# Kernel optimization log

Measured on AMD Instinct MI355X. Metric: run time of the kernel, lower is better.

The kernel has to match this reference:

```python
import jax, jax.numpy as jnp
import numpy as np

# spk_param = (thr, temp, damp); dt, tau from module config
THR, TEMP, DAMP = 0.4, 0.1, 0.9
DT, TAU = 0.1, 1.0


@jax.custom_vjp
def spike(v, u):
    # Stochastic Bernoulli spike: sigmoid(temp*v) > uniform noise
    return (jax.nn.sigmoid(TEMP * v) > u).astype(v.dtype)

def _spike_fwd(v, u):
    return spike(v, u), v

def _spike_bwd(v, g):
    # Faithful to the torch Spike.backward: returns the pseudo-derivative
    # damp*clamp(1-|v|,0) directly (the original ignores grad_output).
    return (DAMP * jnp.maximum(1.0 - jnp.abs(v), 0.0), jnp.zeros_like(v))

spike.defvjp(_spike_fwd, _spike_bwd)


def setup_inputs() -> dict:
    key = jax.random.key(0)
    k1, k2, k3, k4, k5 = jax.random.split(key, 5)
    B_, T, IN, N, OUT = 128, 512, 128, 512, 128
    inputs = jax.random.normal(k1, (B_, T, IN), dtype=jnp.float32)
    rand_u = jax.random.uniform(k2, (B_, T, N), dtype=jnp.float32)
    init_std = 1.0
    J = jax.random.normal(k3, (N, N), dtype=jnp.float32) * (init_std / np.sqrt(N))
    Bw = jax.random.normal(k4, (N, IN), dtype=jnp.float32)  # input projection (non-trainable in torch)
    W = jax.random.normal(k5, (OUT, N), dtype=jnp.float32) * (1.0 / np.sqrt(N))
    return {"inputs": inputs, "rand_u": rand_u, "J": J, "Bw": Bw, "W": W}


def reference(inputs, rand_u, J, Bw, W):
    B_, T, _ = inputs.shape
    N = J.shape[0]
    alpha = DT / TAU
    decay = 1.0 - alpha

    def step(carry, xs):
        v, z = carry
        x_t, u_t = xs  # [B, IN], [B, N]
        v_new = decay * v + alpha * z
        lamb = jnp.tanh(v_new) @ J.T + x_t @ Bw.T  # [B, N]
        z_new = spike((lamb - THR) / THR, u_t)
        out = lamb @ W.T  # [B, OUT]
        return (v_new, z_new), (v_new, z_new, out)

    v0 = jnp.zeros((B_, N), dtype=inputs.dtype)
    z0 = jnp.zeros((B_, N), dtype=inputs.dtype)
    xs = (jnp.swapaxes(inputs, 0, 1), jnp.swapaxes(rand_u, 0, 1))  # time-major
    _, (vs, zs, outs) = jax.lax.scan(step, (v0, z0), xs)

    vt = jnp.concatenate([v0[:, None, :], jnp.swapaxes(vs, 0, 1)], axis=1)  # [B, T+1, N]
    zt = jnp.concatenate([z0[:, None, :], jnp.swapaxes(zs, 0, 1)], axis=1)  # [B, T+1, N]
    output_seq = jnp.swapaxes(outs, 0, 1)  # [B, T, OUT]
    return vt, zt, output_seq
```

## Files before the change

### kernel.cpp

```cpp
#include <hip/hip_runtime.h>


typedef __attribute__((ext_vector_type(8))) short short8x;
typedef __attribute__((ext_vector_type(4))) float f32x4;
typedef __attribute__((ext_vector_type(4))) int i32x4;

#define OFF_JQK  (0u)
#define OFF_BWH  (262144u)
#define OFF_BWL  (393216u)
#define OFF_G    (524288u)
#define OFF_M    (786432u)
#define OFF_GPK  (851968u)
#define OFF_MPK  (983040u)

#define SC_J 640.0f
#define SC_S 166.0f

__device__ __forceinline__ unsigned short f2bf(float f) {
  union { float f; unsigned u; } a; a.f = f;
  unsigned r = a.u + 0x7FFFu + ((a.u >> 16) & 1u);
  return (unsigned short)(r >> 16);
}
__device__ __forceinline__ float bf2f(unsigned short h) {
  union { unsigned u; float f; } a; a.u = ((unsigned)h) << 16;
  return a.f;
}
__device__ __forceinline__ float thr_of(float u) {
  return __builtin_fmaf(4.0f, __logf(u / (1.0f - u)), 0.4f);
}
__device__ __forceinline__ float fast_tanh_pos(float x) {
  const float e2 = __expf(x + x);
  return 1.0f - 2.0f / (e2 + 1.0f);
}
__device__ __forceinline__ int sdot4(unsigned a, unsigned b, int acc) {
#if __has_builtin(__builtin_amdgcn_sdot4)
  return __builtin_amdgcn_sdot4((int)a, (int)b, acc, false);
#else
  int r;
  asm("v_dot4_i32_i8 %0, %1, %2, %3" : "=v"(r) : "v"(a), "v"(b), "v"(acc));
  return r;
#endif
}

__launch_bounds__(512)
__global__ void jwm_kernel(const float* __restrict__ J, const float* __restrict__ Bw,
                           const float* __restrict__ W, unsigned char* __restrict__ ws) {
  __shared__ float wrow[512];
  const int o = blockIdx.x;
  const int tid = threadIdx.x;
  wrow[tid] = W[(size_t)o * 512 + tid];
  __syncthreads();
  const int k = tid;
  const int i = tid & 127;
  float g = 0.0f, m = 0.0f;
  for (int n = 0; n < 512; ++n) {
    const float wv = wrow[n];
    g = __builtin_fmaf(wv, J[(size_t)n * 512 + k], g);
    m = __builtin_fmaf(wv, Bw[(size_t)n * 128 + i], m);
  }
  ((float*)(ws + OFF_G))[(size_t)o * 512 + k] = g;
  if (tid < 128) ((float*)(ws + OFF_M))[(size_t)o * 128 + i] = m;
}

__global__ void pack_kernel(const float* __restrict__ J, const float* __restrict__ Bw,
                            unsigned char* __restrict__ ws) {
  const int id = blockIdx.x * 256 + threadIdx.x;
  if (id < 16384) {
    const int idx = id;
    const int n = idx & 511, kg = idx >> 9, k0 = kg * 16;
    unsigned dw[4];
#pragma unroll
    for (int d = 0; d < 4; ++d) {
      unsigned x = 0;
#pragma unroll
      for (int p = 0; p < 4; ++p) {
        const float jv = J[(size_t)n * 512 + k0 + 4 * d + p];
        int q = __float2int_rn(jv * SC_J);
        q = q > 127 ? 127 : (q < -127 ? -127 : q);
        x |= ((unsigned)(q & 255)) << (8 * p);
      }
      dw[d] = x;
    }
    uint4 out; out.x = dw[0]; out.y = dw[1]; out.z = dw[2]; out.w = dw[3];
    ((uint4*)(ws + OFF_JQK))[idx] = out;
  } else if (id < 24576) {
    const int idx = id - 16384;
    const int n = idx & 511, kg = idx >> 9, k0 = kg * 8;
    unsigned short* bwh = (unsigned short*)(ws + OFF_BWH);
    unsigned short* bwl = (unsigned short*)(ws + OFF_BWL);
    for (int e = 0; e < 8; ++e) {
      const float x = Bw[(size_t)n * 128 + k0 + e];
      const unsigned short h = f2bf(x);
      bwh[(size_t)idx * 8 + e] = h;
      bwl[(size_t)idx * 8 + e] = f2bf(x - bf2f(h));
    }
  } else if (id < 32768) {
    const int idx = id - 24576;
    const int o = idx & 127, kg = idx >> 7, k0 = kg * 8;
    const float* G = (const float*)(ws + OFF_G);
    unsigned short* gpk = (unsigned short*)(ws + OFF_GPK);
    for (int e = 0; e < 8; ++e) gpk[(size_t)idx * 8 + e] = f2bf(G[(size_t)o * 512 + k0 + e]);
  } else {
    const int idx = id - 32768;
    const int o = idx & 127, kg = idx >> 7, k0 = kg * 8;
    const float* M = (const float*)(ws + OFF_M);
    unsigned short* mpk = (unsigned short*)(ws + OFF_MPK);
    for (int e = 0; e < 8; ++e) mpk[(size_t)idx * 8 + e] = f2bf(M[(size_t)o * 128 + k0 + e]);
  }
}

__launch_bounds__(256)
__global__ void xpd_kernel(const float* __restrict__ X, const float* __restrict__ U,
                           const unsigned char* __restrict__ ws, float* __restrict__ Dbuf) {
  __shared__ short Ah[64 * 136];
  __shared__ short Al[64 * 136];
  const unsigned short* bwh = (const unsigned short*)(ws + OFF_BWH);
  const unsigned short* bwl = (const unsigned short*)(ws + OFF_BWL);
  const int m0 = blockIdx.x * 64;
  const int n0 = blockIdx.y * 64;
  const int tid = threadIdx.x;
  for (int i = tid; i < 64 * 32; i += 256) {
    const int r = i >> 5, kq = i & 31;
    const float4 x4 = *(const float4*)(X + (size_t)(m0 + r) * 128 + kq * 4);
    short4 h4, l4; unsigned short h;
    h = f2bf(x4.x); h4.x = (short)h; l4.x = (short)f2bf(x4.x - bf2f(h));
    h = f2bf(x4.y); h4.y = (short)h; l4.y = (short)f2bf(x4.y - bf2f(h));
    h = f2bf(x4.z); h4.z = (short)h; l4.z = (short)f2bf(x4.z - bf2f(h));
    h = f2bf(x4.w); h4.w = (short)h; l4.w = (short)f2bf(x4.w - bf2f(h));
    *(short4*)(&Ah[r * 136 + kq * 4]) = h4;
    *(short4*)(&Al[r * 136 + kq * 4]) = l4;
  }
  __syncthreads();
  const int w = tid >> 6, l = tid & 63, lhi = l >> 4, llo = l & 15;
  const int rowA = 16 * w + llo;
  f32x4 a0 = {0,0,0,0}, a1 = {0,0,0,0}, a2 = {0,0,0,0}, a3 = {0,0,0,0};
#pragma unroll
  for (int kt = 0; kt < 4; ++kt) {
    const short8x ah = *(const short8x*)(&Ah[rowA * 136 + kt * 32 + lhi * 8]);
    const short8x al = *(const short8x*)(&Al[rowA * 136 + kt * 32 + lhi * 8]);
#define XT(TI, ACC) { \
    const size_t bi = ((size_t)((kt * 4 + lhi) * 512 + n0 + TI * 16 + llo)) * 8; \
    const short8x bh = *(const short8x*)(bwh + bi); \
    const short8x bl = *(const short8x*)(bwl + bi); \
    ACC = __builtin_amdgcn_mfma_f32_16x16x32_bf16(ah, bh, ACC, 0, 0, 0); \
    ACC = __builtin_amdgcn_mfma_f32_16x16x32_bf16(al, bh, ACC, 0, 0, 0); \
    ACC = __builtin_amdgcn_mfma_f32_16x16x32_bf16(ah, bl, ACC, 0, 0, 0); }
    XT(0, a0) XT(1, a1) XT(2, a2) XT(3, a3)
#undef XT
  }
  const int n = n0 + llo;
#pragma unroll
  for (int r = 0; r < 4; ++r) {
    const int bt = m0 + 16 * w + lhi * 4 + r;
    const float* urow = U + (size_t)bt * 512;
    float* drow = Dbuf + (size_t)bt * 512;
    drow[n]      = thr_of(urow[n])      - a0[r];
    drow[n + 16] = thr_of(urow[n + 16]) - a1[r];
    drow[n + 32] = thr_of(urow[n + 32]) - a2[r];
    drow[n + 48] = thr_of(urow[n + 48]) - a3[r];
  }
}

__launch_bounds__(512, 1)
__global__ void recur_kernel(const unsigned char* __restrict__ ws,
                             const float* __restrict__ Dbuf,
                             unsigned char* __restrict__ z8) {
  __shared__ __align__(16) unsigned char s_sm[2][512];
  const int b = blockIdx.x;
  const int tid = threadIdx.x;

  uint4 jr[32];
#pragma unroll
  for (int kg = 0; kg < 32; ++kg) {
    const unsigned char* p = ws + OFF_JQK + ((size_t)kg * 512 + (size_t)tid) * 16;
    asm volatile("global_load_dwordx4 %0, %1, off" : "=v"(jr[kg]) : "v"(p));
  }
  asm volatile("s_waitcnt vmcnt(0)" ::: "memory");

  const float SC = 1.0f / (SC_J * SC_S);
  const float* Dp = Dbuf + (size_t)b * 262144 + tid;
  unsigned char* zwg = z8 + (size_t)b * 262144 + tid;

  float dc[8], dnx[8];
#pragma unroll
  for (int i = 0; i < 8; ++i) dc[i] = Dp[(size_t)i * 512];

  unsigned zprev = 0u;
  float v0 = 0.0f, v1 = 0.1f;
  unsigned q0 = (unsigned)__float2int_rn(fast_tanh_pos(v0) * SC_S);
  unsigned q1 = (unsigned)__float2int_rn(fast_tanh_pos(v1) * SC_S);

  for (int c = 0; c < 64; ++c) {
    const int t0 = c * 8;
#pragma unroll
    for (int i = 0; i < 8; ++i) dnx[i] = Dp[(size_t)(t0 + 8 + i) * 512];
#pragma unroll
    for (int i = 0; i < 8; ++i) {
      const int t = t0 + i;
      const unsigned q = zprev ? q1 : q0;
      const float v = zprev ? v1 : v0;
      s_sm[t & 1][tid] = (unsigned char)q;
      asm volatile("s_waitcnt lgkmcnt(0)\n\ts_barrier" ::: "memory");
      v0 = 0.9f * v; v1 = v0 + 0.1f;
      q0 = (unsigned)__float2int_rn(fast_tanh_pos(v0) * SC_S);
      q1 = (unsigned)__float2int_rn(fast_tanh_pos(v1) * SC_S);
      const uint4* sp = (const uint4*)s_sm[t & 1];
      int a0 = 0, a1 = 0, a2 = 0, a3 = 0;
#pragma unroll
      for (int g = 0; g < 32; ++g) {
        const uint4 sv = sp[g];
        a0 = sdot4(jr[g].x, sv.x, a0);
        a1 = sdot4(jr[g].y, sv.y, a1);
        a2 = sdot4(jr[g].z, sv.z, a2);
        a3 = sdot4(jr[g].w, sv.w, a3);
      }
      const float lam = (float)((a0 + a1) + (a2 + a3)) * SC;
      const unsigned z = (lam > dc[i]) ? 1u : 0u;
      zwg[(size_t)t * 512] = (unsigned char)z;
      zprev = z;
    }
#pragma unroll
    for (int i = 0; i < 8; ++i) dc[i] = dnx[i];
  }
}

__launch_bounds__(512)
__global__ void vsz_kernel(const float* __restrict__ X, const unsigned char* __restrict__ ws,
                           float* __restrict__ vt, float* __restrict__ zt,
                           float* __restrict__ op) {
  __shared__ unsigned zl[8192];
  __shared__ unsigned short sl[64 * 520];
  __shared__ unsigned short xl[64 * 136];
  const int b = blockIdx.x;
  const int tid = threadIdx.x;
  const int w = tid >> 6, l = tid & 63, lhi = l >> 4, llo = l & 15;
  const unsigned short* gpk = (const unsigned short*)(ws + OFF_GPK);
  const unsigned short* mpk = (const unsigned short*)(ws + OFF_MPK);
  const unsigned char* z8 = (const unsigned char*)op;

  float v = 0.0f;
  unsigned zprev = 0u;
  vt[((size_t)b * 513) * 512 + tid] = 0.0f;
  zt[((size_t)b * 513) * 512 + tid] = 0.0f;

  for (int c = 0; c < 8; ++c) {
    const uint4* src = (const uint4*)(z8 + (size_t)b * 262144 + (size_t)c * 32768);
#pragma unroll
    for (int i = 0; i < 4; ++i) ((uint4*)zl)[i * 512 + tid] = src[i * 512 + tid];
#pragma unroll
    for (int i = 0; i < 4; ++i) {
      const int idx = i * 512 + tid;
      const int r = idx >> 5, c4 = (idx & 31) * 4;
      const float4 x4 = *(const float4*)(X + ((size_t)b * 512 + c * 64 + r) * 128 + c4);
      short4 h4;
      h4.x = (short)f2bf(x4.x); h4.y = (short)f2bf(x4.y);
      h4.z = (short)f2bf(x4.z); h4.w = (short)f2bf(x4.w);
      *(short4*)(xl + r * 136 + c4) = h4;
    }
    __syncthreads();
    const unsigned char* zb = (const unsigned char*)zl;
    float* vrow = vt + ((size_t)b * 513 + c * 64 + 1) * 512 + tid;
    float* zrow = zt + ((size_t)b * 513 + c * 64 + 1) * 512 + tid;
#pragma unroll 8
    for (int tl = 0; tl < 64; ++tl) {
      v = __builtin_fmaf(0.9f, v, zprev ? 0.1f : 0.0f);
      const unsigned z = zb[tl * 512 + tid];
      vrow[(size_t)tl * 512] = v;
      zrow[(size_t)tl * 512] = z ? 1.0f : 0.0f;
      sl[tl * 520 + tid] = f2bf(fast_tanh_pos(v));
      zprev = z;
    }
    __syncthreads();
    const int m = w >> 1, oh = (w & 1) * 4;
    f32x4 a0 = {0,0,0,0}, a1 = {0,0,0,0}, a2 = {0,0,0,0}, a3 = {0,0,0,0};
#pragma unroll
    for (int kt = 0; kt < 16; ++kt) {
      const short8x A = *(const short8x*)(sl + (m * 16 + llo) * 520 + kt * 32 + lhi * 8);
#define GT(TI, ACC) { \
      const short8x B = *(const short8x*)(gpk + ((size_t)((kt * 4 + lhi) * 128 + (oh + TI) * 16 + llo)) * 8); \
      ACC = __builtin_amdgcn_mfma_f32_16x16x32_bf16(A, B, ACC, 0, 0, 0); }
      GT(0, a0) GT(1, a1) GT(2, a2) GT(3, a3)
#undef GT
    }
#pragma unroll
    for (int kt = 0; kt < 4; ++kt) {
      const short8x A = *(const short8x*)(xl + (m * 16 + llo) * 136 + kt * 32 + lhi * 8);
#define MT(TI, ACC) { \
      const short8x B = *(const short8x*)(mpk + ((size_t)((kt * 4 + lhi) * 128 + (oh + TI) * 16 + llo)) * 8); \
      ACC = __builtin_amdgcn_mfma_f32_16x16x32_bf16(A, B, ACC, 0, 0, 0); }
      MT(0, a0) MT(1, a1) MT(2, a2) MT(3, a3)
#undef MT
    }
    float* obase = op + ((size_t)b * 512 + c * 64 + m * 16 + lhi * 4) * 128 + llo;
#pragma unroll
    for (int r = 0; r < 4; ++r) {
      float* orow = obase + (size_t)r * 128;
      orow[(oh + 0) * 16] = a0[r];
      orow[(oh + 1) * 16] = a1[r];
      orow[(oh + 2) * 16] = a2[r];
      orow[(oh + 3) * 16] = a3[r];
    }
    __syncthreads();
  }
}

extern "C" void kernel_launch(void* const* d_in, const int* in_sizes, int n_in,
                              void* d_out, int out_size, void* d_ws, size_t ws_size,
                              hipStream_t stream) {
  const float* X  = (const float*)d_in[0];
  const float* U  = (const float*)d_in[1];
  const float* J  = (const float*)d_in[2];
  const float* Bw = (const float*)d_in[3];
  const float* W  = (const float*)d_in[4];
  float* vt = (float*)d_out;
  float* zt = vt + (size_t)128 * 513 * 512;
  float* op = vt + (size_t)2 * 128 * 513 * 512;
  unsigned char* ws = (unsigned char*)d_ws;
  float* Dbuf = vt;
  unsigned char* z8 = (unsigned char*)op;

  jwm_kernel<<<128, 512, 0, stream>>>(J, Bw, W, ws);
  pack_kernel<<<136, 256, 0, stream>>>(J, Bw, ws);
  xpd_kernel<<<dim3(1024, 8), 256, 0, stream>>>(X, U, ws, Dbuf);
  recur_kernel<<<128, 512, 0, stream>>>(ws, Dbuf, z8);
  vsz_kernel<<<128, 512, 0, stream>>>(X, ws, vt, zt, op);
}
```

Baseline: 824.3 us.

## Split recurrent dot product across 8 lanes with DPP reduction to cut LDS reads

```diff
diff --git a/kernel.cpp b/kernel.cpp
--- a/kernel.cpp
+++ b/kernel.cpp
@@ -40,6 +40,13 @@
   asm("v_dot4_i32_i8 %0, %1, %2, %3" : "=v"(r) : "v"(a), "v"(b), "v"(acc));
   return r;
 #endif
+}
+template <int CTRL>
+__device__ __forceinline__ int dpp_add(int x) {
+  return x + __builtin_amdgcn_update_dpp(0, x, CTRL, 0xF, 0xF, true);
+}
+__device__ __forceinline__ int dpp_reduce8(int x) {
+  return dpp_add<0x141>(dpp_add<0x4E>(dpp_add<0xB1>(x)));
 }
 
 __launch_bounds__(512)
@@ -66,8 +73,12 @@
                             unsigned char* __restrict__ ws) {
   const int id = blockIdx.x * 256 + threadIdx.x;
   if (id < 16384) {
-    const int idx = id;
-    const int n = idx & 511, kg = idx >> 9, k0 = kg * 16;
+    const int f = id;
+    const int l = f & 63, j = (f >> 6) & 3, i = (f >> 8) & 7, w = f >> 11;
+    const int kap = l & 7;
+    const int n = w * 64 + (l >> 3) * 8 + i;
+    const int c = (j + kap) & 3;
+    const int k0 = 64 * kap + 16 * c;
     unsigned dw[4];
 #pragma unroll
     for (int d = 0; d < 4; ++d) {
@@ -82,7 +93,7 @@
       dw[d] = x;
     }
     uint4 out; out.x = dw[0]; out.y = dw[1]; out.z = dw[2]; out.w = dw[3];
-    ((uint4*)(ws + OFF_JQK))[idx] = out;
+    ((uint4*)(ws + OFF_JQK))[f] = out;
   } else if (id < 24576) {
     const int idx = id - 16384;
     const int n = idx & 511, kg = idx >> 9, k0 = kg * 8;
@@ -168,14 +179,24 @@
   __shared__ __align__(16) unsigned char s_sm[2][512];
   const int b = blockIdx.x;
   const int tid = threadIdx.x;
-
-  uint4 jr[32];
-#pragma unroll
-  for (int kg = 0; kg < 32; ++kg) {
-    const unsigned char* p = ws + OFF_JQK + ((size_t)kg * 512 + (size_t)tid) * 16;
-    asm volatile("global_load_dwordx4 %0, %1, off" : "=v"(jr[kg]) : "v"(p));
-  }
+  const int w = tid >> 6, l = tid & 63;
+  const int kap = l & 7;
+
+  uint4 jr[8][4];
+#pragma unroll
+  for (int i = 0; i < 8; ++i)
+#pragma unroll
+    for (int j = 0; j < 4; ++j) {
+      const unsigned char* p = ws + OFF_JQK +
+          (size_t)(((w * 8 + i) * 4 + j) * 64 + l) * 16;
+      asm volatile("global_load_dwordx4 %0, %1, off" : "=v"(jr[i][j]) : "v"(p));
+    }
   asm volatile("s_waitcnt vmcnt(0)" ::: "memory");
+
+  const int o0 = kap * 64 + (((0 + kap) & 3) << 4);
+  const int o1 = kap * 64 + (((1 + kap) & 3) << 4);
+  const int o2 = kap * 64 + (((2 + kap) & 3) << 4);
+  const int o3 = kap * 64 + (((3 + kap) & 3) << 4);
 
   const float SC = 1.0f / (SC_J * SC_S);
   const float* Dp = Dbuf + (size_t)b * 262144 + tid;
@@ -204,17 +225,40 @@
       v0 = 0.9f * v; v1 = v0 + 0.1f;
       q0 = (unsigned)__float2int_rn(fast_tanh_pos(v0) * SC_S);
       q1 = (unsigned)__float2int_rn(fast_tanh_pos(v1) * SC_S);
-      const uint4* sp = (const uint4*)s_sm[t & 1];
-      int a0 = 0, a1 = 0, a2 = 0, a3 = 0;
-#pragma unroll
-      for (int g = 0; g < 32; ++g) {
-        const uint4 sv = sp[g];
-        a0 = sdot4(jr[g].x, sv.x, a0);
-        a1 = sdot4(jr[g].y, sv.y, a1);
-        a2 = sdot4(jr[g].z, sv.z, a2);
-        a3 = sdot4(jr[g].w, sv.w, a3);
-      }
-      const float lam = (float)((a0 + a1) + (a2 + a3)) * SC;
+      const unsigned char* sb = &s_sm[t & 1][0];
+      const uint4 s0 = *(const uint4*)(sb + o0);
+      const uint4 s1 = *(const uint4*)(sb + o1);
+      const uint4 s2 = *(const uint4*)(sb + o2);
+      const uint4 s3 = *(const uint4*)(sb + o3);
+      int a0 = 0, a1 = 0, a2 = 0, a3 = 0, a4 = 0, a5 = 0, a6 = 0, a7 = 0;
+#define DOT(AI, I) \
+      AI = sdot4(jr[I][0].x, s0.x, AI); AI = sdot4(jr[I][0].y, s0.y, AI); \
+      AI = sdot4(jr[I][0].z, s0.z, AI); AI = sdot4(jr[I][0].w, s0.w, AI); \
+      AI = sdot4(jr[I][1].x, s1.x, AI); AI = sdot4(jr[I][1].y, s1.y, AI); \
+      AI = sdot4(jr[I][1].z, s1.z, AI); AI = sdot4(jr[I][1].w, s1.w, AI); \
+      AI = sdot4(jr[I][2].x, s2.x, AI); AI = sdot4(jr[I][2].y, s2.y, AI); \
+      AI = sdot4(jr[I][2].z, s2.z, AI); AI = sdot4(jr[I][2].w, s2.w, AI); \
+      AI = sdot4(jr[I][3].x, s3.x, AI); AI = sdot4(jr[I][3].y, s3.y, AI); \
+      AI = sdot4(jr[I][3].z, s3.z, AI); AI = sdot4(jr[I][3].w, s3.w, AI);
+      DOT(a0, 0) DOT(a1, 1) DOT(a2, 2) DOT(a3, 3)
+      DOT(a4, 4) DOT(a5, 5) DOT(a6, 6) DOT(a7, 7)
+#undef DOT
+      a0 = dpp_reduce8(a0);
+      a1 = dpp_reduce8(a1);
+      a2 = dpp_reduce8(a2);
+      a3 = dpp_reduce8(a3);
+      a4 = dpp_reduce8(a4);
+      a5 = dpp_reduce8(a5);
+      a6 = dpp_reduce8(a6);
+      a7 = dpp_reduce8(a7);
+      const int q01 = (l & 1) ? a1 : a0;
+      const int q23 = (l & 1) ? a3 : a2;
+      const int q45 = (l & 1) ? a5 : a4;
+      const int q67 = (l & 1) ? a7 : a6;
+      const int r0 = (l & 2) ? q23 : q01;
+      const int r1 = (l & 2) ? q67 : q45;
+      const int accv = (l & 4) ? r1 : r0;
+      const float lam = (float)accv * SC;
       const unsigned z = (lam > dc[i]) ? 1u : 0u;
       zwg[(size_t)t * 512] = (unsigned char)z;
       zprev = z;
```

Measured after the change: 812.1 us. Within noise of the previous version (-1.5%).

## Fuse recurrence and output kernels with flag-based producer/consumer overlap

Applied to the files above, without the earlier changes.

```diff
diff --git a/kernel.cpp b/kernel.cpp
--- a/kernel.cpp
+++ b/kernel.cpp
@@ -3,7 +3,6 @@
 
 typedef __attribute__((ext_vector_type(8))) short short8x;
 typedef __attribute__((ext_vector_type(4))) float f32x4;
-typedef __attribute__((ext_vector_type(4))) int i32x4;
 
 #define OFF_JQK  (0u)
 #define OFF_BWH  (262144u)
@@ -12,6 +11,7 @@
 #define OFF_M    (786432u)
 #define OFF_GPK  (851968u)
 #define OFF_MPK  (983040u)
+#define OFF_FLG  (1048576u)
 
 #define SC_J 640.0f
 #define SC_S 166.0f
@@ -32,14 +32,12 @@
   const float e2 = __expf(x + x);
   return 1.0f - 2.0f / (e2 + 1.0f);
 }
-__device__ __forceinline__ int sdot4(unsigned a, unsigned b, int acc) {
-#if __has_builtin(__builtin_amdgcn_sdot4)
-  return __builtin_amdgcn_sdot4((int)a, (int)b, acc, false);
-#else
-  int r;
-  asm("v_dot4_i32_i8 %0, %1, %2, %3" : "=v"(r) : "v"(a), "v"(b), "v"(acc));
-  return r;
-#endif
+__device__ __forceinline__ void sdot4a(int& acc, unsigned a, unsigned b) {
+  asm("v_dot4_i32_i8 %0, %1, %2, %0" : "+v"(acc) : "v"(a), "v"(b));
+}
+template <int CTRL>
+__device__ __forceinline__ int dppmov(int x) {
+  return __builtin_amdgcn_update_dpp(0, x, CTRL, 0xF, 0xF, true);
 }
 
 __launch_bounds__(512)
@@ -50,8 +48,7 @@
   const int tid = threadIdx.x;
   wrow[tid] = W[(size_t)o * 512 + tid];
   __syncthreads();
-  const int k = tid;
-  const int i = tid & 127;
+  const int k = tid, i = tid & 127;
   float g = 0.0f, m = 0.0f;
   for (int n = 0; n < 512; ++n) {
     const float wv = wrow[n];
@@ -65,9 +62,13 @@
 __global__ void pack_kernel(const float* __restrict__ J, const float* __restrict__ Bw,
                             unsigned char* __restrict__ ws) {
   const int id = blockIdx.x * 256 + threadIdx.x;
+  if (id < 128) ((unsigned*)(ws + OFF_FLG))[id] = 0u;
   if (id < 16384) {
-    const int idx = id;
-    const int n = idx & 511, kg = idx >> 9, k0 = kg * 16;
+    const int f = id;
+    const int l = f & 63, j = (f >> 6) & 3, i = (f >> 8) & 7, w = f >> 11;
+    const int kap = l & 7;
+    const int n = w * 64 + (l >> 3) * 8 + i;
+    const int k0 = 64 * kap + 16 * j;
     unsigned dw[4];
 #pragma unroll
     for (int d = 0; d < 4; ++d) {
@@ -82,7 +83,7 @@
       dw[d] = x;
     }
     uint4 out; out.x = dw[0]; out.y = dw[1]; out.z = dw[2]; out.w = dw[3];
-    ((uint4*)(ws + OFF_JQK))[idx] = out;
+    ((uint4*)(ws + OFF_JQK))[f] = out;
   } else if (id < 24576) {
     const int idx = id - 16384;
     const int n = idx & 511, kg = idx >> 9, k0 = kg * 8;
@@ -152,8 +153,9 @@
 #pragma unroll
   for (int r = 0; r < 4; ++r) {
     const int bt = m0 + 16 * w + lhi * 4 + r;
+    const int bb = bt >> 9, tt = bt & 511;
     const float* urow = U + (size_t)bt * 512;
-    float* drow = Dbuf + (size_t)bt * 512;
+    float* drow = Dbuf + ((size_t)bb * 513 + tt + 1) * 512;
     drow[n]      = thr_of(urow[n])      - a0[r];
     drow[n + 16] = thr_of(urow[n + 16]) - a1[r];
     drow[n + 32] = thr_of(urow[n + 32]) - a2[r];
@@ -162,145 +164,180 @@
 }
 
 __launch_bounds__(512, 1)
-__global__ void recur_kernel(const unsigned char* __restrict__ ws,
-                             const float* __restrict__ Dbuf,
-                             unsigned char* __restrict__ z8) {
-  __shared__ __align__(16) unsigned char s_sm[2][512];
-  const int b = blockIdx.x;
-  const int tid = threadIdx.x;
-
-  uint4 jr[32];
-#pragma unroll
-  for (int kg = 0; kg < 32; ++kg) {
-    const unsigned char* p = ws + OFF_JQK + ((size_t)kg * 512 + (size_t)tid) * 16;
-    asm volatile("global_load_dwordx4 %0, %1, off" : "=v"(jr[kg]) : "v"(p));
-  }
-  asm volatile("s_waitcnt vmcnt(0)" ::: "memory");
-
-  const float SC = 1.0f / (SC_J * SC_S);
-  const float* Dp = Dbuf + (size_t)b * 262144 + tid;
-  unsigned char* zwg = z8 + (size_t)b * 262144 + tid;
-
-  float dc[8], dnx[8];
-#pragma unroll
-  for (int i = 0; i < 8; ++i) dc[i] = Dp[(size_t)i * 512];
-
-  unsigned zprev = 0u;
-  float v0 = 0.0f, v1 = 0.1f;
-  unsigned q0 = (unsigned)__float2int_rn(fast_tanh_pos(v0) * SC_S);
-  unsigned q1 = (unsigned)__float2int_rn(fast_tanh_pos(v1) * SC_S);
-
-  for (int c = 0; c < 64; ++c) {
-    const int t0 = c * 8;
-#pragma unroll
-    for (int i = 0; i < 8; ++i) dnx[i] = Dp[(size_t)(t0 + 8 + i) * 512];
-#pragma unroll
-    for (int i = 0; i < 8; ++i) {
-      const int t = t0 + i;
-      const unsigned q = zprev ? q1 : q0;
-      const float v = zprev ? v1 : v0;
-      s_sm[t & 1][tid] = (unsigned char)q;
-      asm volatile("s_waitcnt lgkmcnt(0)\n\ts_barrier" ::: "memory");
-      v0 = 0.9f * v; v1 = v0 + 0.1f;
-      q0 = (unsigned)__float2int_rn(fast_tanh_pos(v0) * SC_S);
-      q1 = (unsigned)__float2int_rn(fast_tanh_pos(v1) * SC_S);
-      const uint4* sp = (const uint4*)s_sm[t & 1];
-      int a0 = 0, a1 = 0, a2 = 0, a3 = 0;
-#pragma unroll
-      for (int g = 0; g < 32; ++g) {
-        const uint4 sv = sp[g];
-        a0 = sdot4(jr[g].x, sv.x, a0);
-        a1 = sdot4(jr[g].y, sv.y, a1);
-        a2 = sdot4(jr[g].z, sv.z, a2);
-        a3 = sdot4(jr[g].w, sv.w, a3);
-      }
-      const float lam = (float)((a0 + a1) + (a2 + a3)) * SC;
-      const unsigned z = (lam > dc[i]) ? 1u : 0u;
-      zwg[(size_t)t * 512] = (unsigned char)z;
-      zprev = z;
-    }
-#pragma unroll
-    for (int i = 0; i < 8; ++i) dc[i] = dnx[i];
-  }
-}
-
-__launch_bounds__(512)
-__global__ void vsz_kernel(const float* __restrict__ X, const unsigned char* __restrict__ ws,
-                           float* __restrict__ vt, float* __restrict__ zt,
-                           float* __restrict__ op) {
+__global__ void fused_kernel(const float* __restrict__ X, unsigned char* __restrict__ ws,
+                             float* __restrict__ vt, float* __restrict__ zt,
+                             float* __restrict__ op) {
+  __shared__ __align__(16) unsigned char s_sm[2][640];
   __shared__ unsigned zl[8192];
   __shared__ unsigned short sl[64 * 520];
   __shared__ unsigned short xl[64 * 136];
-  const int b = blockIdx.x;
+  unsigned* flags = (unsigned*)(ws + OFF_FLG);
   const int tid = threadIdx.x;
-  const int w = tid >> 6, l = tid & 63, lhi = l >> 4, llo = l & 15;
-  const unsigned short* gpk = (const unsigned short*)(ws + OFF_GPK);
-  const unsigned short* mpk = (const unsigned short*)(ws + OFF_MPK);
-  const unsigned char* z8 = (const unsigned char*)op;
-
-  float v = 0.0f;
-  unsigned zprev = 0u;
-  vt[((size_t)b * 513) * 512 + tid] = 0.0f;
-  zt[((size_t)b * 513) * 512 + tid] = 0.0f;
-
-  for (int c = 0; c < 8; ++c) {
-    const uint4* src = (const uint4*)(z8 + (size_t)b * 262144 + (size_t)c * 32768);
-#pragma unroll
-    for (int i = 0; i < 4; ++i) ((uint4*)zl)[i * 512 + tid] = src[i * 512 + tid];
-#pragma unroll
-    for (int i = 0; i < 4; ++i) {
-      const int idx = i * 512 + tid;
-      const int r = idx >> 5, c4 = (idx & 31) * 4;
-      const float4 x4 = *(const float4*)(X + ((size_t)b * 512 + c * 64 + r) * 128 + c4);
-      short4 h4;
-      h4.x = (short)f2bf(x4.x); h4.y = (short)f2bf(x4.y);
-      h4.z = (short)f2bf(x4.z); h4.w = (short)f2bf(x4.w);
-      *(short4*)(xl + r * 136 + c4) = h4;
+
+  if (blockIdx.x < 128) {
+    const int b = blockIdx.x;
+    const int w = tid >> 6, l = tid & 63;
+    const int kap = l & 7, kap80 = kap * 80;
+
+    uint4 jr[8][4];
+#pragma unroll
+    for (int i = 0; i < 8; ++i)
+#pragma unroll
+      for (int j = 0; j < 4; ++j) {
+        const unsigned char* p = ws + OFF_JQK +
+            (size_t)(((w * 8 + i) * 4 + j) * 64 + l) * 16;
+        asm volatile("global_load_dwordx4 %0, %1, off" : "=v"(jr[i][j]) : "v"(p));
+      }
+    asm volatile("s_waitcnt vmcnt(0)" ::: "memory");
+
+    const float SC = 1.0f / (SC_J * SC_S);
+    const float* Dp = vt + ((size_t)b * 513 + 1) * 512 + tid;
+    unsigned char* zwg = (unsigned char*)op + (size_t)b * 262144 + tid;
+    unsigned* flagp = flags + b;
+
+    float dc[8], dnx[8];
+#pragma unroll
+    for (int i = 0; i < 8; ++i) dc[i] = Dp[(size_t)i * 512];
+
+    unsigned zprev = 0u;
+    float v0 = 0.0f, v1 = 0.1f;
+    unsigned q0 = (unsigned)__float2int_rn(fast_tanh_pos(v0) * SC_S);
+    unsigned q1 = (unsigned)__float2int_rn(fast_tanh_pos(v1) * SC_S);
+
+    for (int c = 0; c < 64; ++c) {
+      const int t0 = c * 8;
+#pragma unroll
+      for (int i = 0; i < 8; ++i) dnx[i] = Dp[(size_t)(t0 + 8 + i) * 512];
+#pragma unroll
+      for (int i = 0; i < 8; ++i) {
+        const int t = t0 + i;
+        const unsigned q = zprev ? q1 : q0;
+        const float v = zprev ? v1 : v0;
+        s_sm[t & 1][w * 80 + l] = (unsigned char)q;
+        asm volatile("s_waitcnt lgkmcnt(0)\n\ts_barrier" ::: "memory");
+        v0 = 0.9f * v; v1 = v0 + 0.1f;
+        q0 = (unsigned)__float2int_rn(fast_tanh_pos(v0) * SC_S);
+        q1 = (unsigned)__float2int_rn(fast_tanh_pos(v1) * SC_S);
+        const unsigned char* sb = &s_sm[t & 1][0];
+        const uint4 s0 = *(const uint4*)(sb + kap80);
+        const uint4 s1 = *(const uint4*)(sb + kap80 + 16);
+        const uint4 s2 = *(const uint4*)(sb + kap80 + 32);
+        const uint4 s3 = *(const uint4*)(sb + kap80 + 48);
+        int a0 = 0, a1 = 0, a2 = 0, a3 = 0, a4 = 0, a5 = 0, a6 = 0, a7 = 0;
+#define DOT(AI, I) \
+        sdot4a(AI, jr[I][0].x, s0.x); sdot4a(AI, jr[I][0].y, s0.y); \
+        sdot4a(AI, jr[I][0].z, s0.z); sdot4a(AI, jr[I][0].w, s0.w); \
+        sdot4a(AI, jr[I][1].x, s1.x); sdot4a(AI, jr[I][1].y, s1.y); \
+        sdot4a(AI, jr[I][1].z, s1.z); sdot4a(AI, jr[I][1].w, s1.w); \
+        sdot4a(AI, jr[I][2].x, s2.x); sdot4a(AI, jr[I][2].y, s2.y); \
+        sdot4a(AI, jr[I][2].z, s2.z); sdot4a(AI, jr[I][2].w, s2.w); \
+        sdot4a(AI, jr[I][3].x, s3.x); sdot4a(AI, jr[I][3].y, s3.y); \
+        sdot4a(AI, jr[I][3].z, s3.z); sdot4a(AI, jr[I][3].w, s3.w);
+        DOT(a0, 0) DOT(a1, 1) DOT(a2, 2) DOT(a3, 3)
+        DOT(a4, 4) DOT(a5, 5) DOT(a6, 6) DOT(a7, 7)
+#undef DOT
+        const bool b1 = (l & 1), b2 = (l & 2), b4 = (l & 4);
+        int x0 = b1 ? a1 : a0, y0 = b1 ? a0 : a1; x0 += dppmov<0xB1>(y0);
+        int x1 = b1 ? a3 : a2, y1 = b1 ? a2 : a3; x1 += dppmov<0xB1>(y1);
+        int x2 = b1 ? a5 : a4, y2 = b1 ? a4 : a5; x2 += dppmov<0xB1>(y2);
+        int x3 = b1 ? a7 : a6, y3 = b1 ? a6 : a7; x3 += dppmov<0xB1>(y3);
+        int u0 = b2 ? x1 : x0, w0 = b2 ? x0 : x1; u0 += dppmov<0x4E>(w0);
+        int u1 = b2 ? x3 : x2, w1 = b2 ? x2 : x3; u1 += dppmov<0x4E>(w1);
+        int own  = b4 ? u1 : u0;
+        const int send = b4 ? u0 : u1;
+        own += __builtin_amdgcn_ds_swizzle(send, 0x101F);
+        const float lam = (float)own * SC;
+        const unsigned z = (lam > dc[i]) ? 1u : 0u;
+        zwg[(size_t)t * 512] = (unsigned char)z;
+        zprev = z;
+      }
+      if ((c & 3) == 3)
+        __hip_atomic_store(flagp, (unsigned)(t0 + 8), __ATOMIC_RELEASE,
+                           __HIP_MEMORY_SCOPE_AGENT);
+#pragma unroll
+      for (int i = 0; i < 8; ++i) dc[i] = dnx[i];
     }
-    __syncthreads();
-    const unsigned char* zb = (const unsigned char*)zl;
-    float* vrow = vt + ((size_t)b * 513 + c * 64 + 1) * 512 + tid;
-    float* zrow = zt + ((size_t)b * 513 + c * 64 + 1) * 512 + tid;
+  } else {
+    const int b = blockIdx.x - 128;
+    const int w = tid >> 6, l = tid & 63, lhi = l >> 4, llo = l & 15;
+    const unsigned short* gpk = (const unsigned short*)(ws + OFF_GPK);
+    const unsigned short* mpk = (const unsigned short*)(ws + OFF_MPK);
+    const unsigned char* z8 = (const unsigned char*)op;
+    const unsigned* flagp = flags + b;
+
+    float v = 0.0f;
+    unsigned zprev = 0u;
+    vt[((size_t)b * 513) * 512 + tid] = 0.0f;
+    zt[((size_t)b * 513) * 512 + tid] = 0.0f;
+
+    for (int c = 0; c < 8; ++c) {
+      {
+        const unsigned tgt = (unsigned)(64 * (c + 1));
+        long guard = 0;
+        while (__hip_atomic_load(flagp, __ATOMIC_ACQUIRE,
+                                 __HIP_MEMORY_SCOPE_AGENT) < tgt) {
+          __builtin_amdgcn_s_sleep(8);
+          if (++guard > 200000000L) break;
+        }
+      }
+      const uint4* src = (const uint4*)(z8 + (size_t)b * 262144 + (size_t)c * 32768);
+#pragma unroll
+      for (int i = 0; i < 4; ++i) ((uint4*)zl)[i * 512 + tid] = src[i * 512 + tid];
+#pragma unroll
+      for (int i = 0; i < 4; ++i) {
+        const int idx = i * 512 + tid;
+        const int r = idx >> 5, c4 = (idx & 31) * 4;
+        const float4 x4 = *(const float4*)(X + ((size_t)b * 512 + c * 64 + r) * 128 + c4);
+        short4 h4;
+        h4.x = (short)f2bf(x4.x); h4.y = (short)f2bf(x4.y);
+        h4.z = (short)f2bf(x4.z); h4.w = (short)f2bf(x4.w);
+        *(short4*)(xl + r * 136 + c4) = h4;
+      }
+      __syncthreads();
+      const unsigned char* zb = (const unsigned char*)zl;
+      float* vrow = vt + ((size_t)b * 513 + c * 64 + 1) * 512 + tid;
+      float* zrow = zt + ((size_t)b * 513 + c * 64 + 1) * 512 + tid;
 #pragma unroll 8
-    for (int tl = 0; tl < 64; ++tl) {
-      v = __builtin_fmaf(0.9f, v, zprev ? 0.1f : 0.0f);
-      const unsigned z = zb[tl * 512 + tid];
-      vrow[(size_t)tl * 512] = v;
-      zrow[(size_t)tl * 512] = z ? 1.0f : 0.0f;
-      sl[tl * 520 + tid] = f2bf(fast_tanh_pos(v));
-      zprev = z;
+      for (int tl = 0; tl < 64; ++tl) {
+        v = __builtin_fmaf(0.9f, v, zprev ? 0.1f : 0.0f);
+        const unsigned z = zb[tl * 512 + tid];
+        vrow[(size_t)tl * 512] = v;
+        zrow[(size_t)tl * 512] = z ? 1.0f : 0.0f;
+        sl[tl * 520 + tid] = f2bf(fast_tanh_pos(v));
+        zprev = z;
+      }
+      __syncthreads();
+      const int m = w >> 1, oh = (w & 1) * 4;
+      f32x4 a0 = {0,0,0,0}, a1 = {0,0,0,0}, a2 = {0,0,0,0}, a3 = {0,0,0,0};
+#pragma unroll
+      for (int kt = 0; kt < 16; ++kt) {
+        const short8x A = *(const short8x*)(sl + (m * 16 + llo) * 520 + kt * 32 + lhi * 8);
+#define GT(TI, ACC) { \
+        const short8x B = *(const short8x*)(gpk + ((size_t)((kt * 4 + lhi) * 128 + (oh + TI) * 16 + llo)) * 8); \
+        ACC = __builtin_amdgcn_mfma_f32_16x16x32_bf16(A, B, ACC, 0, 0, 0); }
+        GT(0, a0) GT(1, a1) GT(2, a2) GT(3, a3)
+#undef GT
+      }
+#pragma unroll
+      for (int kt = 0; kt < 4; ++kt) {
+        const short8x A = *(const short8x*)(xl + (m * 16 + llo) * 136 + kt * 32 + lhi * 8);
+#define MT(TI, ACC) { \
+        const short8x B = *(const short8x*)(mpk + ((size_t)((kt * 4 + lhi) * 128 + (oh + TI) * 16 + llo)) * 8); \
+        ACC = __builtin_amdgcn_mfma_f32_16x16x32_bf16(A, B, ACC, 0, 0, 0); }
+        MT(0, a0) MT(1, a1) MT(2, a2) MT(3, a3)
+#undef MT
+      }
+      float* obase = op + ((size_t)b * 512 + c * 64 + m * 16 + lhi * 4) * 128 + llo;
+#pragma unroll
+      for (int r = 0; r < 4; ++r) {
+        float* orow = obase + (size_t)r * 128;
+        orow[(oh + 0) * 16] = a0[r];
+        orow[(oh + 1) * 16] = a1[r];
+        orow[(oh + 2) * 16] = a2[r];
+        orow[(oh + 3) * 16] = a3[r];
+      }
+      __syncthreads();
     }
-    __syncthreads();
-    const int m = w >> 1, oh = (w & 1) * 4;
-    f32x4 a0 = {0,0,0,0}, a1 = {0,0,0,0}, a2 = {0,0,0,0}, a3 = {0,0,0,0};
-#pragma unroll
-    for (int kt = 0; kt < 16; ++kt) {
-      const short8x A = *(const short8x*)(sl + (m * 16 + llo) * 520 + kt * 32 + lhi * 8);
-#define GT(TI, ACC) { \
-      const short8x B = *(const short8x*)(gpk + ((size_t)((kt * 4 + lhi) * 128 + (oh + TI) * 16 + llo)) * 8); \
-      ACC = __builtin_amdgcn_mfma_f32_16x16x32_bf16(A, B, ACC, 0, 0, 0); }
-      GT(0, a0) GT(1, a1) GT(2, a2) GT(3, a3)
-#undef GT
-    }
-#pragma unroll
-    for (int kt = 0; kt < 4; ++kt) {
-      const short8x A = *(const short8x*)(xl + (m * 16 + llo) * 136 + kt * 32 + lhi * 8);
-#define MT(TI, ACC) { \
-      const short8x B = *(const short8x*)(mpk + ((size_t)((kt * 4 + lhi) * 128 + (oh + TI) * 16 + llo)) * 8); \
-      ACC = __builtin_amdgcn_mfma_f32_16x16x32_bf16(A, B, ACC, 0, 0, 0); }
-      MT(0, a0) MT(1, a1) MT(2, a2) MT(3, a3)
-#undef MT
-    }
-    float* obase = op + ((size_t)b * 512 + c * 64 + m * 16 + lhi * 4) * 128 + llo;
-#pragma unroll
-    for (int r = 0; r < 4; ++r) {
-      float* orow = obase + (size_t)r * 128;
-      orow[(oh + 0) * 16] = a0[r];
-      orow[(oh + 1) * 16] = a1[r];
-      orow[(oh + 2) * 16] = a2[r];
-      orow[(oh + 3) * 16] = a3[r];
-    }
-    __syncthreads();
   }
 }
 
@@ -316,12 +353,9 @@
   float* zt = vt + (size_t)128 * 513 * 512;
   float* op = vt + (size_t)2 * 128 * 513 * 512;
   unsigned char* ws = (unsigned char*)d_ws;
-  float* Dbuf = vt;
-  unsigned char* z8 = (unsigned char*)op;
 
   jwm_kernel<<<128, 512, 0, stream>>>(J, Bw, W, ws);
   pack_kernel<<<136, 256, 0, stream>>>(J, Bw, ws);
-  xpd_kernel<<<dim3(1024, 8), 256, 0, stream>>>(X, U, ws, Dbuf);
-  recur_kernel<<<128, 512, 0, stream>>>(ws, Dbuf, z8);
-  vsz_kernel<<<128, 512, 0, stream>>>(X, ws, vt, zt, op);
-}
+  xpd_kernel<<<dim3(1024, 8), 256, 0, stream>>>(X, U, ws, vt);
+  fused_kernel<<<256, 512, 0, stream>>>(X, ws, vt, zt, op);
+}
```

Result: slower. 946.3 us (+14.8%).
